# Optimization experiments

Hardware: AMD Instinct MI355X
Metric: run time of the kernel (lower is better)

The kernel has to match this reference:

```python
import jax, jax.numpy as jnp
import numpy as np

V, EMB, HID, ENC = 32000, 512, 1024, 1024
B, T, TB = 64, 512, 512
PAD = 0


def setup_inputs() -> dict:
    key = jax.random.key(0)
    kk = jax.random.split(key, 24)
    w = lambda k, s: jax.random.normal(k, s, dtype=jnp.float32) * 0.02
    a = lambda k, s: jax.random.normal(k, s, dtype=jnp.float32)
    emb_table = w(kk[0], (V, EMB)).at[PAD].set(0.0)  # padding_idx row zeroed
    IN = EMB + ENC + HID  # lstm input size
    return {
        "y": jax.random.randint(kk[1], (B,), 0, V),
        "h": a(kk[2], (B, HID)),
        "c": a(kk[3], (B, HID)),
        "enc_out": a(kk[4], (B, T, ENC)),
        "bwd_states": a(kk[5], (B, TB, HID)),
        "src_ids": jax.random.randint(kk[6], (B, T), 0, V),
        "src_mask": jnp.ones((B, T), dtype=jnp.int32),
        "emb_table": emb_table,
        "W_ih": w(kk[7], (4 * HID, IN)),
        "W_hh": w(kk[8], (4 * HID, HID)),
        "b_ih": jnp.zeros((4 * HID,), jnp.float32),
        "b_hh": jnp.zeros((4 * HID,), jnp.float32),
        "Wq_e": w(kk[9], (HID, HID)),
        "Wk_e": w(kk[10], (HID, ENC)),
        "v_e": w(kk[11], (HID,)),
        "Wq_b": w(kk[12], (HID, HID)),
        "Wk_b": w(kk[13], (HID, HID)),
        "v_b": w(kk[14], (HID,)),
        "Wp": w(kk[15], (V, HID)),
        "bp": jnp.zeros((V,), jnp.float32),
        "wc": w(kk[16], (ENC,)),
        "ws": w(kk[17], (HID,)),
        "wy": w(kk[18], (EMB,)),
        "pg_b": jnp.zeros((), jnp.float32),
    }


def _bahdanau(query, keys, Wq, Wk, v, mask=None):
    # query [B,H], keys [B,T,D] -> context [B,D], attn [B,T]
    q = query @ Wq.T                                  # [B,A]
    k = jnp.einsum("btd,ad->bta", keys, Wk)           # [B,T,A]
    e = jnp.einsum("bta,a->bt", jnp.tanh(q[:, None, :] + k), v)
    if mask is not None:
        e = jnp.where(mask == 0, jnp.finfo(e.dtype).min, e)
    attn = jax.nn.softmax(e, axis=-1)
    ctx = jnp.einsum("bt,btd->bd", attn, keys)
    return ctx, attn


def reference(y, h, c, enc_out, bwd_states, src_ids, src_mask, emb_table,
              W_ih, W_hh, b_ih, b_hh, Wq_e, Wk_e, v_e, Wq_b, Wk_b, v_b,
              Wp, bp, wc, ws, wy, pg_b):
    emb = emb_table[y]                                # [B,EMB]
    query = h                                         # state[0].squeeze(0)
    c_enc, attn_enc = _bahdanau(query, enc_out, Wq_e, Wk_e, v_e, src_mask)
    c_bwd, _ = _bahdanau(query, bwd_states, Wq_b, Wk_b, v_b)
    x = jnp.concatenate([emb, c_enc, c_bwd], axis=-1)  # [B,EMB+ENC+HID]
    gates = x @ W_ih.T + h @ W_hh.T + b_ih + b_hh      # [B,4H], torch order i,f,g,o
    i, f, g, o = jnp.split(gates, 4, axis=-1)
    c_new = jax.nn.sigmoid(f) * c + jax.nn.sigmoid(i) * jnp.tanh(g)
    h_new = jax.nn.sigmoid(o) * jnp.tanh(c_new)
    vocab_dist = jax.nn.softmax(h_new @ Wp.T + bp, axis=-1)  # [B,V]
    p_gen = jax.nn.sigmoid(c_enc @ wc + h_new @ ws + emb @ wy + pg_b)[:, None]
    p_vocab = p_gen * vocab_dist
    copy_mask = (src_ids < V).astype(vocab_dist.dtype)
    safe_ids = jnp.minimum(src_ids, V - 1)
    contrib = (1.0 - p_gen) * attn_enc * copy_mask     # [B,T]
    scatter = jax.vmap(lambda idx, val: jnp.zeros((V,), val.dtype).at[idx].add(val))(safe_ids, contrib)
    final_dist = p_vocab + scatter
    return final_dist, h_new, c_new
```

## Files before the change

kernel.cpp:

```cpp
#include <hip/hip_runtime.h>
#include <hip/hip_bf16.h>

#define VSZ   32000
#define EMBD  512
#define HIDD  1024
#define BB    64
#define TSEQ  512
#define G4    4096

typedef short bf16x8 __attribute__((ext_vector_type(8)));
typedef float f32x4  __attribute__((ext_vector_type(4)));

typedef __attribute__((address_space(3))) unsigned       lds_u32_t;
typedef __attribute__((address_space(1))) const unsigned glb_u32_t;
__device__ __forceinline__ void gload16(const void* g, void* l){
  __builtin_amdgcn_global_load_lds((glb_u32_t*)g, (lds_u32_t*)l, 16, 0, 0);
}

__device__ __forceinline__ float sigmoid_f(float x){ return 1.0f/(1.0f+__expf(-x)); }
__device__ __forceinline__ float fast_tanh(float x){
  float e = __expf(2.0f*x);
  return 1.0f - 2.0f*__builtin_amdgcn_rcpf(e + 1.0f);
}
__device__ __forceinline__ short f2bfs(float x){
  unsigned u = __float_as_uint(x);
  unsigned r = (u + 0x7FFFu + ((u>>16)&1u)) >> 16;
  return (short)r;
}
__device__ __forceinline__ float bf2f(short s){
  return __uint_as_float(((unsigned)(unsigned short)s) << 16);
}
__device__ __forceinline__ unsigned cvtpk(float a, float b){
  unsigned r;
  asm("v_cvt_pk_bf16_f32 %0, %1, %2" : "=v"(r) : "v"(a), "v"(b));
  return r;
}
__device__ __forceinline__ bf16x8 cvt8(float4 a, float4 b){
  union { unsigned u[4]; bf16x8 v; } o;
  o.u[0]=cvtpk(a.x,a.y); o.u[1]=cvtpk(a.z,a.w);
  o.u[2]=cvtpk(b.x,b.y); o.u[3]=cvtpk(b.z,b.w);
  return o.v;
}
__device__ __forceinline__ float wave_sum(float x){
  #pragma unroll
  for (int off=32; off>0; off>>=1) x += __shfl_xor(x, off);
  return x;
}
__device__ __forceinline__ float wave_max(float x){
  #pragma unroll
  for (int off=32; off>0; off>>=1) x = fmaxf(x, __shfl_xor(x, off));
  return x;
}

__global__ __launch_bounds__(256) void k_prep_all(
    const float* __restrict__ Wk_e, const float* __restrict__ Wk_b,
    const float* __restrict__ enc,  const float* __restrict__ bwd,
    const float* __restrict__ h,
    const float* __restrict__ tab,  const int* __restrict__ y,
    short* __restrict__ pk_e, short* __restrict__ pk_b,
    short* __restrict__ pkeys, short* __restrict__ xb){
  int bid = blockIdx.x;
  if (bid < 1024){
    const float* Wk = (bid < 512) ? Wk_e : Wk_b;
    short* dst      = (bid < 512) ? pk_e : pk_b;
    int id = (bid & 511)*256 + threadIdx.x;
    int a = id >> 7, g = id & 127;
    int gs = (g & ~7) | ((g & 7) ^ (a & 7));
    const float* src = Wk + (size_t)a*1024 + gs*8;
    float4 f0 = ((const float4*)src)[0], f1 = ((const float4*)src)[1];
    *(bf16x8*)(dst + (size_t)id*8) = cvt8(f0, f1);
  } else if (bid < 33792){
    int r = bid - 1024;
    int att = r >> 14;
    const float* src0 = att ? bwd : enc;
    int id = (r & 16383)*256 + threadIdx.x;
    int g = id & 127, bt = id >> 7;
    int t = bt & 511;
    int gs = (g & ~7) | ((g & 7) ^ (t & 7));
    const float* sp = src0 + (size_t)bt*1024 + gs*8;
    float4 f0 = ((const float4*)sp)[0], f1 = ((const float4*)sp)[1];
    *(bf16x8*)(pkeys + (((size_t)att*32768 + bt)*128 + g)*8) = cvt8(f0, f1);
  } else if (bid < 33824){
    int id = (bid - 33792)*256 + threadIdx.x;
    int b = id >> 7, d = (id & 127)*8;
    const float4* s = (const float4*)(h + (size_t)b*HIDD + d);
    *(bf16x8*)(xb + (size_t)b*3584 + 2560 + d) = cvt8(s[0], s[1]);
  } else {
    int id = (bid - 33824)*256 + threadIdx.x;
    int b = id >> 6, d = (id & 63)*8;
    const float* src = tab + (size_t)y[b]*EMBD + d;
    float4 f0 = ((const float4*)src)[0], f1 = ((const float4*)src)[1];
    *(bf16x8*)(xb + (size_t)b*3584 + d) = cvt8(f0, f1);
  }
}

__global__ __launch_bounds__(256) void k_mm64(
    const short* __restrict__ A0, int lda0, const float* __restrict__ B0, int ldb0, int K0, float* __restrict__ out0, int ldo0,
    const short* __restrict__ A1, int lda1, const float* __restrict__ B1, int ldb1, int K1, float* __restrict__ out1, int ldo1){
  const short* A; const float* B; float* out; int lda, ldb, K, ldo;
  if (blockIdx.z == 0){ A=A0; B=B0; out=out0; lda=lda0; ldb=ldb0; K=K0; ldo=ldo0; }
  else                { A=A1; B=B1; out=out1; lda=lda1; ldb=ldb1; K=K1; ldo=ldo1; }
  int tid = threadIdx.x, l = tid & 63, w = tid >> 6;
  int l15 = l & 15, l4 = l >> 4;
  int n0 = blockIdx.x*256 + w*64;
  int kper = K / gridDim.y;
  int dbeg = blockIdx.y * kper, dend = dbeg + kper;
  f32x4 acc[4][4];
  #pragma unroll
  for (int i=0;i<4;i++)
    #pragma unroll
    for (int j=0;j<4;j++)
      #pragma unroll
      for (int r=0;r<4;r++) acc[i][j][r]=0.f;
  for (int d0=dbeg; d0<dend; d0+=32){
    bf16x8 af[4];
    #pragma unroll
    for (int ms=0; ms<4; ms++)
      af[ms] = *(const bf16x8*)(A + (size_t)(ms*16 + l15)*lda + d0 + l4*8);
    bf16x8 bfr[4];
    #pragma unroll
    for (int ni=0; ni<4; ni++){
      const float* bp = B + (size_t)(n0 + ni*16 + l15)*ldb + d0 + l4*8;
      float4 f0 = ((const float4*)bp)[0], f1 = ((const float4*)bp)[1];
      bfr[ni] = cvt8(f0, f1);
    }
    #pragma unroll
    for (int ms=0; ms<4; ms++)
      #pragma unroll
      for (int ni=0; ni<4; ni++)
        acc[ms][ni] = __builtin_amdgcn_mfma_f32_16x16x32_bf16(af[ms], bfr[ni], acc[ms][ni], 0,0,0);
  }
  float* op = out + (size_t)blockIdx.y * 64 * ldo;
  #pragma unroll
  for (int ms=0; ms<4; ms++)
    #pragma unroll
    for (int ni=0; ni<4; ni++)
      #pragma unroll
      for (int r=0; r<4; r++){
        int m = ms*16 + l4*4 + r;
        op[(size_t)m*ldo + n0 + ni*16 + l15] = acc[ms][ni][r];
      }
}

__global__ __launch_bounds__(256,3) void k_energy(
    const short* __restrict__ pkeys,
    const short* __restrict__ pke, const short* __restrict__ pkb,
    const float* __restrict__ qpe, const float* __restrict__ qpb,
    const float* __restrict__ ve, const float* __restrict__ vb,
    float* __restrict__ ep_out){
  __shared__ short A_s[128*64];
  __shared__ short B_s[128*64];
  __shared__ float ebuf[2][128];

  int wg = blockIdx.x;
  int xcd = wg & 7, idx = wg >> 3;
  int tglob = xcd*64 + (idx >> 3);
  int A0 = idx & 7;
  int att = tglob >> 8;
  int tt  = tglob & 255;
  int b = tt >> 2, t0 = (tt & 3)*128;

  const short* pk = att ? pkb : pke;
  const float* qp = att ? qpb : qpe;
  const float* v  = att ? vb  : ve;

  int tid = threadIdx.x, l = tid & 63, w = tid >> 6;
  int l15 = l & 15, l4 = l >> 4;
  int wr = w >> 1, wc = w & 1;

  const char* asrc = (const char*)(pkeys + ((size_t)att*32768 + (size_t)b*512)*1024)
                   + (size_t)(t0 + w*32 + (l>>3))*2048 + (l&7)*16;
  const char* bsrc = (const char*)pk + (size_t)(A0*128 + w*32 + (l>>3))*2048 + (l&7)*16;

  f32x4 acc[4][4];
  #pragma unroll
  for (int i=0;i<4;i++)
    #pragma unroll
    for (int j=0;j<4;j++)
      #pragma unroll
      for (int r=0;r<4;r++) acc[i][j][r]=0.f;

  for (int c=0; c<16; ++c){
    if (c) __syncthreads();
    #pragma unroll
    for (int k=0;k<4;k++)
      gload16(asrc + (size_t)c*128 + (size_t)k*16384, (char*)A_s + w*4096 + k*1024);
    #pragma unroll
    for (int k=0;k<4;k++)
      gload16(bsrc + (size_t)c*128 + (size_t)k*16384, (char*)B_s + w*4096 + k*1024);
    __syncthreads();
    #pragma unroll
    for (int ks=0; ks<2; ks++){
      bf16x8 af[4], bf[4];
      #pragma unroll
      for (int ms=0; ms<4; ms++){
        int row = wr*64 + ms*16 + l15;
        af[ms] = *(const bf16x8*)((char*)A_s + row*128 + ((ks*64 + l4*16) ^ ((row&7)<<4)));
      }
      #pragma unroll
      for (int ni=0; ni<4; ni++){
        int row = wc*64 + ni*16 + l15;
        bf[ni] = *(const bf16x8*)((char*)B_s + row*128 + ((ks*64 + l4*16) ^ ((row&7)<<4)));
      }
      #pragma unroll
      for (int ms=0; ms<4; ms++)
        #pragma unroll
        for (int ni=0; ni<4; ni++)
          acc[ms][ni] = __builtin_amdgcn_mfma_f32_16x16x32_bf16(af[ms], bf[ni], acc[ms][ni], 0,0,0);
    }
  }

  float qv[4], vv[4];
  #pragma unroll
  for (int ni=0; ni<4; ni++){
    int a = A0*128 + wc*64 + ni*16 + l15;
    float q = 0.f;
    #pragma unroll
    for (int s=0; s<8; s++) q += qp[(size_t)s*65536 + (size_t)b*HIDD + a];
    qv[ni] = q;
    vv[ni] = v[a];
  }
  float es[16];
  #pragma unroll
  for (int ms=0; ms<4; ms++)
    #pragma unroll
    for (int r=0; r<4; r++){
      float s = 0.f;
      #pragma unroll
      for (int ni=0; ni<4; ni++)
        s += vv[ni]*fast_tanh(qv[ni] + acc[ms][ni][r]);
      es[ms*4+r] = s;
    }
  #pragma unroll
  for (int i=0;i<16;i++){
    float x = es[i];
    x += __shfl_xor(x,1); x += __shfl_xor(x,2);
    x += __shfl_xor(x,4); x += __shfl_xor(x,8);
    es[i] = x;
  }
  if (l15 == 0){
    #pragma unroll
    for (int ms=0; ms<4; ms++)
      #pragma unroll
      for (int r=0; r<4; r++)
        ebuf[wc][wr*64 + ms*16 + l4*4 + r] = es[ms*4+r];
  }
  __syncthreads();
  if (tid < 128)
    ep_out[(((size_t)att*8 + A0)*BB + b)*TSEQ + t0 + tid] = ebuf[0][tid] + ebuf[1][tid];
}

__global__ __launch_bounds__(256) void k_softmax_t(const float* __restrict__ ep,
                                                   const int* __restrict__ mask,
                                                   float* __restrict__ att_e,
                                                   float* __restrict__ att_b){
  int b = blockIdx.x, att = blockIdx.y;
  float* e = (att ? att_b : att_e) + (size_t)b*TSEQ;
  __shared__ float red[8];
  int tid = threadIdx.x, lane = tid & 63, w = tid >> 6;
  float v0 = 0.f, v1 = 0.f;
  #pragma unroll
  for (int i=0;i<8;i++){
    const float* p = ep + (((size_t)att*8 + i)*BB + b)*TSEQ;
    v0 += p[tid]; v1 += p[tid+256];
  }
  if (att==0){
    if (mask[(size_t)b*TSEQ + tid]==0)      v0 = -3.4e38f;
    if (mask[(size_t)b*TSEQ + tid+256]==0)  v1 = -3.4e38f;
  }
  float m = wave_max(fmaxf(v0, v1));
  if (lane==0) red[w] = m;
  __syncthreads();
  m = fmaxf(fmaxf(red[0],red[1]), fmaxf(red[2],red[3]));
  float x0 = __expf(v0-m), x1 = __expf(v1-m);
  float s = wave_sum(x0+x1);
  if (lane==0) red[4+w] = s;
  __syncthreads();
  s = red[4]+red[5]+red[6]+red[7];
  float inv = 1.0f/s;
  e[tid] = x0*inv; e[tid+256] = x1*inv;
}

__global__ __launch_bounds__(256) void k_ctx(const short* __restrict__ pkeys,
                                             const float* __restrict__ att_e,
                                             const float* __restrict__ att_b,
                                             float* __restrict__ ctxp){
  int b = blockIdx.x, sel = blockIdx.y, s = blockIdx.z;
  const short* base = pkeys + (((size_t)sel*32768) + (size_t)b*512 + s*64)*1024;
  const float* att  = (sel ? att_b : att_e) + (size_t)b*TSEQ + s*64;
  int g = threadIdx.x & 127, th = threadIdx.x >> 7;
  const short* rp = base + (size_t)th*32*1024;
  float acc[8];
  #pragma unroll
  for (int j=0;j<8;j++) acc[j]=0.f;
  for (int t=0;t<32;t++){
    float a = att[th*32 + t];
    int gg = (g & ~7) | ((g & 7) ^ (t & 7));
    bf16x8 kv = *(const bf16x8*)(rp + (size_t)t*1024 + gg*8);
    #pragma unroll
    for (int j=0;j<8;j++) acc[j] += a*bf2f(kv[j]);
  }
  float* o = ctxp + ((((size_t)sel*BB + b)*16) + s*2 + th)*1024 + g*8;
  float4 o0, o1;
  o0.x=acc[0]; o0.y=acc[1]; o0.z=acc[2]; o0.w=acc[3];
  o1.x=acc[4]; o1.y=acc[5]; o1.z=acc[6]; o1.w=acc[7];
  ((float4*)o)[0] = o0; ((float4*)o)[1] = o1;
}

__global__ __launch_bounds__(256) void k_ctxred(const float* __restrict__ ctxp,
                                                float* __restrict__ ctx_e,
                                                short* __restrict__ xb){
  int id = blockIdx.x*256 + threadIdx.x;
  int sel = id >> 16; int rem = id & 65535; int b = rem >> 10; int d = rem & 1023;
  const float* p = ctxp + (((size_t)sel*BB + b)*16)*1024 + d;
  float s = 0.f;
  #pragma unroll
  for (int i=0;i<16;i++) s += p[i*1024];
  if (sel==0) ctx_e[(size_t)b*HIDD + d] = s;
  xb[(size_t)b*3584 + 512 + sel*1024 + d] = f2bfs(s);
}

__global__ __launch_bounds__(256) void k_lstm(const float* __restrict__ gp,
                                              const float* __restrict__ b_ih,
                                              const float* __restrict__ b_hh,
                                              const float* __restrict__ c_old,
                                              float* __restrict__ out,
                                              short* __restrict__ hb){
  int id = blockIdx.x*256 + threadIdx.x;
  int b = id >> 10, j = id & 1023;
  size_t base = (size_t)b*G4;
  float gs[4];
  #pragma unroll
  for (int g=0; g<4; g++){
    int col = g*1024 + j;
    float s = b_ih[col] + b_hh[col];
    #pragma unroll
    for (int k=0;k<16;k++) s += gp[(size_t)k*(64*G4) + base + col];
    gs[g] = s;
  }
  float ig = sigmoid_f(gs[0]);
  float fg = sigmoid_f(gs[1]);
  float gg = tanhf(gs[2]);
  float og = sigmoid_f(gs[3]);
  float cn = fg*c_old[id] + ig*gg;
  float hn = og*tanhf(cn);
  out[(size_t)BB*VSZ + id] = hn;
  out[(size_t)BB*VSZ + (size_t)BB*HIDD + id] = cn;
  hb[id] = f2bfs(hn);
}

__global__ __launch_bounds__(256) void k_vocab2(const short* __restrict__ hb,
                                                const float* __restrict__ Wp,
                                                const float* __restrict__ bp,
                                                float* __restrict__ out){
  int tid = threadIdx.x, l = tid & 63, w = tid >> 6;
  int l15 = l & 15, l4 = l >> 4;
  int mh = w >> 1;
  int n0 = blockIdx.x*128 + (w&1)*64;
  f32x4 acc[2][4];
  #pragma unroll
  for (int i=0;i<2;i++)
    #pragma unroll
    for (int j=0;j<4;j++)
      #pragma unroll
      for (int r=0;r<4;r++) acc[i][j][r]=0.f;
  #pragma unroll 2
  for (int d0=0; d0<1024; d0+=32){
    bf16x8 af[2];
    #pragma unroll
    for (int ms=0; ms<2; ms++)
      af[ms] = *(const bf16x8*)(hb + (size_t)(mh*32 + ms*16 + l15)*1024 + d0 + l4*8);
    bf16x8 bfr[4];
    #pragma unroll
    for (int ni=0; ni<4; ni++){
      const float* bpp = Wp + (size_t)(n0 + ni*16 + l15)*1024 + d0 + l4*8;
      float4 f0 = ((const float4*)bpp)[0], f1 = ((const float4*)bpp)[1];
      bfr[ni] = cvt8(f0, f1);
    }
    #pragma unroll
    for (int ms=0; ms<2; ms++)
      #pragma unroll
      for (int ni=0; ni<4; ni++)
        acc[ms][ni] = __builtin_amdgcn_mfma_f32_16x16x32_bf16(af[ms], bfr[ni], acc[ms][ni], 0,0,0);
  }
  #pragma unroll
  for (int ms=0; ms<2; ms++)
    #pragma unroll
    for (int ni=0; ni<4; ni++)
      #pragma unroll
      for (int r=0; r<4; r++){
        int m = mh*32 + ms*16 + l4*4 + r;
        int n = n0 + ni*16 + l15;
        out[(size_t)m*VSZ + n] = acc[ms][ni][r] + bp[n];
      }
}

__global__ __launch_bounds__(256) void k_vred(const float* __restrict__ out,
                                              const float* __restrict__ ctxe,
                                              const float* __restrict__ tab,
                                              const int* __restrict__ y,
                                              const float* __restrict__ wc,
                                              const float* __restrict__ wsv,
                                              const float* __restrict__ wy,
                                              const float* __restrict__ pgb,
                                              float* __restrict__ vm,
                                              float* __restrict__ vs,
                                              float* __restrict__ pgen_ws){
  __shared__ float red[8];
  int b = blockIdx.x, seg = blockIdx.y;
  int tid = threadIdx.x, lane = tid & 63, w = tid >> 6;
  if (seg < 4){
    const float* row = out + (size_t)b*VSZ;
    int lo = seg*8000, hi = lo + 8000;
    float m = -3.4e38f;
    for (int i=lo+tid; i<hi; i+=256) m = fmaxf(m, row[i]);
    m = wave_max(m);
    if (lane==0) red[w] = m;
    __syncthreads();
    m = fmaxf(fmaxf(red[0],red[1]), fmaxf(red[2],red[3]));
    float s = 0.f;
    for (int i=lo+tid; i<hi; i+=256) s += __expf(row[i]-m);
    s = wave_sum(s);
    if (lane==0) red[4+w] = s;
    __syncthreads();
    if (tid==0){
      vm[b*4+seg] = m;
      vs[b*4+seg] = red[4]+red[5]+red[6]+red[7];
    }
  } else {
    const float* hn = out + (size_t)BB*VSZ + (size_t)b*HIDD;
    const float* emb = tab + (size_t)y[b]*EMBD;
    float acc = 0.f;
    #pragma unroll
    for (int i=0;i<4;i++){
      int d = i*256 + tid;
      acc += ctxe[(size_t)b*HIDD + d]*wc[d] + hn[d]*wsv[d];
    }
    #pragma unroll
    for (int i=0;i<2;i++){
      int d = i*256 + tid;
      acc += emb[d]*wy[d];
    }
    acc = wave_sum(acc);
    if (lane==0) red[w] = acc;
    __syncthreads();
    if (tid==0)
      pgen_ws[b] = sigmoid_f(red[0]+red[1]+red[2]+red[3] + pgb[0]);
  }
}

__global__ __launch_bounds__(256) void k_vscale(float* __restrict__ out,
                                                const float* __restrict__ vm,
                                                const float* __restrict__ vs,
                                                const float* __restrict__ pgen_ws){
  int b = blockIdx.x, seg = blockIdx.y;
  int tid = threadIdx.x;
  float m0=vm[b*4+0], m1=vm[b*4+1], m2=vm[b*4+2], m3=vm[b*4+3];
  float M = fmaxf(fmaxf(m0,m1), fmaxf(m2,m3));
  float S = vs[b*4+0]*__expf(m0-M) + vs[b*4+1]*__expf(m1-M)
          + vs[b*4+2]*__expf(m2-M) + vs[b*4+3]*__expf(m3-M);
  float scale = pgen_ws[b] / S;
  float* row = out + (size_t)b*VSZ;
  int lo = seg*8000, hi = lo + 8000;
  for (int i=lo+tid; i<hi; i+=256) row[i] = __expf(row[i]-M)*scale;
}

__global__ __launch_bounds__(256) void k_scatter(const int* __restrict__ src_ids,
                                                 const float* __restrict__ att_e,
                                                 const float* __restrict__ pgen_ws,
                                                 float* __restrict__ out){
  int id = blockIdx.x*256 + threadIdx.x;
  int b = id >> 9;
  float pg = pgen_ws[b];
  int sid = src_ids[id];
  float contrib = (1.0f - pg) * att_e[id] * (sid < VSZ ? 1.0f : 0.0f);
  int safe = sid < VSZ-1 ? sid : VSZ-1;
  atomicAdd(&out[(size_t)b*VSZ + safe], contrib);
}

extern "C" void kernel_launch(void* const* d_in, const int* in_sizes, int n_in,
                              void* d_out, int out_size, void* d_ws, size_t ws_size,
                              hipStream_t stream){
  const int*   y     = (const int*)d_in[0];
  const float* h     = (const float*)d_in[1];
  const float* c     = (const float*)d_in[2];
  const float* enc   = (const float*)d_in[3];
  const float* bwd   = (const float*)d_in[4];
  const int*   sids  = (const int*)d_in[5];
  const int*   smask = (const int*)d_in[6];
  const float* tab   = (const float*)d_in[7];
  const float* W_ih  = (const float*)d_in[8];
  const float* W_hh  = (const float*)d_in[9];
  const float* b_ih  = (const float*)d_in[10];
  const float* b_hh  = (const float*)d_in[11];
  const float* Wq_e  = (const float*)d_in[12];
  const float* Wk_e  = (const float*)d_in[13];
  const float* v_e   = (const float*)d_in[14];
  const float* Wq_b  = (const float*)d_in[15];
  const float* Wk_b  = (const float*)d_in[16];
  const float* v_b   = (const float*)d_in[17];
  const float* Wp    = (const float*)d_in[18];
  const float* bp    = (const float*)d_in[19];
  const float* wc    = (const float*)d_in[20];
  const float* wsv   = (const float*)d_in[21];
  const float* wy    = (const float*)d_in[22];
  const float* pgb   = (const float*)d_in[23];
  float* out = (float*)d_out;

  float* W = (float*)d_ws;
  float* ws_qpe  = W; W += 8*BB*HIDD;
  float* ws_qpb  = W; W += 8*BB*HIDD;
  float* ws_ep   = W; W += 2*8*BB*TSEQ;
  float* ws_atte = W; W += BB*TSEQ;
  float* ws_attb = W; W += BB*TSEQ;
  float* ws_ctxe = W; W += BB*HIDD;
  float* ws_ctxp = W; W += 2*BB*16*1024;
  float* ws_pgen = W; W += 64;
  float* ws_vm   = W; W += 256;
  float* ws_vs   = W; W += 256;
  float* ws_gp   = W; W += 16*BB*G4;
  short* xb      = (short*)W; W += (BB*3584)/2;
  short* hb      = (short*)W; W += (BB*HIDD)/2;
  short* pk_e    = (short*)W; W += (HIDD*HIDD)/2;
  short* pk_b    = (short*)W; W += (HIDD*HIDD)/2;
  short* pkeys   = (short*)W; W += (2*BB*TSEQ*HIDD)/2;

  k_prep_all<<<33840, 256, 0, stream>>>(Wk_e, Wk_b, enc, bwd, h, tab, y,
      pk_e, pk_b, pkeys, xb);
  k_mm64<<<dim3(4,8,2), 256, 0, stream>>>(
      xb+2560, 3584, Wq_e, 1024, 1024, ws_qpe, 1024,
      xb+2560, 3584, Wq_b, 1024, 1024, ws_qpb, 1024);
  k_energy<<<4096, 256, 0, stream>>>(pkeys, pk_e, pk_b,
      ws_qpe, ws_qpb, v_e, v_b, ws_ep);
  k_softmax_t<<<dim3(BB,2), 256, 0, stream>>>(ws_ep, smask, ws_atte, ws_attb);
  k_ctx<<<dim3(BB,2,8), 256, 0, stream>>>(pkeys, ws_atte, ws_attb, ws_ctxp);
  k_ctxred<<<512, 256, 0, stream>>>(ws_ctxp, ws_ctxe, xb);
  k_mm64<<<dim3(16,8,2), 256, 0, stream>>>(
      xb,      3584, W_ih, 2560, 2560, ws_gp,             G4,
      xb+2560, 3584, W_hh, 1024, 1024, ws_gp + 8*BB*G4,   G4);
  k_lstm<<<256, 256, 0, stream>>>(ws_gp, b_ih, b_hh, c, out, hb);
  k_vocab2<<<250, 256, 0, stream>>>(hb, Wp, bp, out);
  k_vred<<<dim3(BB,5), 256, 0, stream>>>(out, ws_ctxe, tab, y, wc, wsv, wy, pgb,
      ws_vm, ws_vs, ws_pgen);
  k_vscale<<<dim3(BB,4), 256, 0, stream>>>(out, ws_vm, ws_vs, ws_pgen);
  k_scatter<<<128, 256, 0, stream>>>(sids, ws_atte, ws_pgen, out);
}
```

Baseline: 367.7 us.

## Triple-buffer k_energy with async LDS loads and larger 256x128 tiles

Reworks the attention energy GEMM kernel to use 512-thread blocks covering 256 time rows by 128 attention columns, halving the grid. It adds a three-stage LDS ring fed by direct global-to-LDS loads, with explicit vmcnt waits and one barrier per k-step, so that loads for step k+2 overlap the MFMAs of step k. The goal is to hide global memory latency and to reuse each B tile across more rows. In exchange it uses far more LDS per block (about 144 KB) and runs one block per CU, which lowers occupancy and leaves latency hiding entirely to the hand-written pipeline.

```diff
diff --git a/kernel.cpp b/kernel.cpp
--- a/kernel.cpp
+++ b/kernel.cpp
@@ -142,23 +142,23 @@
       }
 }
 
-__global__ __launch_bounds__(256,3) void k_energy(
+__global__ __launch_bounds__(512,1) void k_energy(
     const short* __restrict__ pkeys,
     const short* __restrict__ pke, const short* __restrict__ pkb,
     const float* __restrict__ qpe, const float* __restrict__ qpb,
     const float* __restrict__ ve, const float* __restrict__ vb,
     float* __restrict__ ep_out){
-  __shared__ short A_s[128*64];
-  __shared__ short B_s[128*64];
-  __shared__ float ebuf[2][128];
+  __shared__ short A_all[3*256*64];
+  __shared__ short B_all[3*128*64];
+  __shared__ float ebuf[2][256];
 
   int wg = blockIdx.x;
   int xcd = wg & 7, idx = wg >> 3;
-  int tglob = xcd*64 + (idx >> 3);
-  int A0 = idx & 7;
-  int att = tglob >> 8;
-  int tt  = tglob & 255;
-  int b = tt >> 2, t0 = (tt & 3)*128;
+  int ntile = idx & 7;
+  int gmt = xcd*32 + (idx >> 3);
+  int att = gmt >> 7;
+  int b   = (gmt >> 1) & 63;
+  int t0  = (gmt & 1) * 256;
 
   const short* pk = att ? pkb : pke;
   const float* qp = att ? qpb : qpe;
@@ -166,11 +166,14 @@
 
   int tid = threadIdx.x, l = tid & 63, w = tid >> 6;
   int l15 = l & 15, l4 = l >> 4;
-  int wr = w >> 1, wc = w & 1;
+  int wm = w >> 1, wn = w & 1;
 
   const char* asrc = (const char*)(pkeys + ((size_t)att*32768 + (size_t)b*512)*1024)
                    + (size_t)(t0 + w*32 + (l>>3))*2048 + (l&7)*16;
-  const char* bsrc = (const char*)pk + (size_t)(A0*128 + w*32 + (l>>3))*2048 + (l&7)*16;
+  const char* bsrc = (const char*)pk + (size_t)(ntile*128 + w*16 + (l>>3))*2048 + (l&7)*16;
+
+  char* Ab = (char*)A_all;
+  char* Bb = (char*)B_all;
 
   f32x4 acc[4][4];
   #pragma unroll
@@ -180,40 +183,67 @@
       #pragma unroll
       for (int r=0;r<4;r++) acc[i][j][r]=0.f;
 
-  for (int c=0; c<16; ++c){
-    if (c) __syncthreads();
-    #pragma unroll
-    for (int k=0;k<4;k++)
-      gload16(asrc + (size_t)c*128 + (size_t)k*16384, (char*)A_s + w*4096 + k*1024);
-    #pragma unroll
-    for (int k=0;k<4;k++)
-      gload16(bsrc + (size_t)c*128 + (size_t)k*16384, (char*)B_s + w*4096 + k*1024);
-    __syncthreads();
-    #pragma unroll
-    for (int ks=0; ks<2; ks++){
-      bf16x8 af[4], bf[4];
-      #pragma unroll
-      for (int ms=0; ms<4; ms++){
-        int row = wr*64 + ms*16 + l15;
-        af[ms] = *(const bf16x8*)((char*)A_s + row*128 + ((ks*64 + l4*16) ^ ((row&7)<<4)));
-      }
-      #pragma unroll
-      for (int ni=0; ni<4; ni++){
-        int row = wc*64 + ni*16 + l15;
-        bf[ni] = *(const bf16x8*)((char*)B_s + row*128 + ((ks*64 + l4*16) ^ ((row&7)<<4)));
-      }
-      #pragma unroll
-      for (int ms=0; ms<4; ms++)
-        #pragma unroll
-        for (int ni=0; ni<4; ni++)
-          acc[ms][ni] = __builtin_amdgcn_mfma_f32_16x16x32_bf16(af[ms], bf[ni], acc[ms][ni], 0,0,0);
-    }
-  }
+#define STAGE(KT, BUF) { \
+    const char* as_ = asrc + (size_t)(KT)*128; \
+    char* ad_ = Ab + (BUF)*32768 + w*4096; \
+    gload16(as_,          ad_); \
+    gload16(as_ + 16384,  ad_ + 1024); \
+    gload16(as_ + 32768,  ad_ + 2048); \
+    gload16(as_ + 49152,  ad_ + 3072); \
+    const char* bs_ = bsrc + (size_t)(KT)*128; \
+    char* bd_ = Bb + (BUF)*16384 + w*2048; \
+    gload16(bs_,          bd_); \
+    gload16(bs_ + 16384,  bd_ + 1024); \
+  }
+
+#define MFMA_PHASE(BUF) { \
+    const char* Abase_ = Ab + (BUF)*32768; \
+    const char* Bbase_ = Bb + (BUF)*16384; \
+    _Pragma("unroll") \
+    for (int ks=0; ks<2; ks++){ \
+      bf16x8 af[4], bf[4]; \
+      _Pragma("unroll") \
+      for (int ms=0; ms<4; ms++){ \
+        int row = wm*64 + ms*16 + l15; \
+        af[ms] = *(const bf16x8*)(Abase_ + row*128 + ((ks*64 + l4*16) ^ ((row&7)<<4))); \
+      } \
+      _Pragma("unroll") \
+      for (int ni=0; ni<4; ni++){ \
+        int row = wn*64 + ni*16 + l15; \
+        bf[ni] = *(const bf16x8*)(Bbase_ + row*128 + ((ks*64 + l4*16) ^ ((row&7)<<4))); \
+      } \
+      _Pragma("unroll") \
+      for (int ms=0; ms<4; ms++) \
+        _Pragma("unroll") \
+        for (int ni=0; ni<4; ni++) \
+          acc[ms][ni] = __builtin_amdgcn_mfma_f32_16x16x32_bf16(af[ms], bf[ni], acc[ms][ni], 0,0,0); \
+    } }
+
+  STAGE(0, 0);
+  STAGE(1, 1);
+  asm volatile("s_waitcnt vmcnt(6)" ::: "memory");
+  __builtin_amdgcn_s_barrier();
+  __builtin_amdgcn_sched_barrier(0);
+
+  int cur = 0, stg = 2;
+  #pragma unroll 1
+  for (int kt = 0; kt < 16; ++kt){
+    if (kt < 14) STAGE(kt+2, stg);
+    MFMA_PHASE(cur);
+    if (kt <= 13) asm volatile("s_waitcnt vmcnt(6)" ::: "memory");
+    else          asm volatile("s_waitcnt vmcnt(0)" ::: "memory");
+    __builtin_amdgcn_s_barrier();
+    __builtin_amdgcn_sched_barrier(0);
+    cur = (cur==2) ? 0 : cur+1;
+    stg = (stg==2) ? 0 : stg+1;
+  }
+#undef STAGE
+#undef MFMA_PHASE
 
   float qv[4], vv[4];
   #pragma unroll
   for (int ni=0; ni<4; ni++){
-    int a = A0*128 + wc*64 + ni*16 + l15;
+    int a = ntile*128 + wn*64 + ni*16 + l15;
     float q = 0.f;
     #pragma unroll
     for (int s=0; s<8; s++) q += qp[(size_t)s*65536 + (size_t)b*HIDD + a];
@@ -243,11 +273,11 @@
     for (int ms=0; ms<4; ms++)
       #pragma unroll
       for (int r=0; r<4; r++)
-        ebuf[wc][wr*64 + ms*16 + l4*4 + r] = es[ms*4+r];
+        ebuf[wn][wm*64 + ms*16 + l4*4 + r] = es[ms*4+r];
   }
   __syncthreads();
-  if (tid < 128)
-    ep_out[(((size_t)att*8 + A0)*BB + b)*TSEQ + t0 + tid] = ebuf[0][tid] + ebuf[1][tid];
+  if (tid < 256)
+    ep_out[(((size_t)att*8 + ntile)*BB + b)*TSEQ + t0 + tid] = ebuf[0][tid] + ebuf[1][tid];
 }
 
 __global__ __launch_bounds__(256) void k_softmax_t(const float* __restrict__ ep,
@@ -530,7 +560,7 @@
   k_mm64<<<dim3(4,8,2), 256, 0, stream>>>(
       xb+2560, 3584, Wq_e, 1024, 1024, ws_qpe, 1024,
       xb+2560, 3584, Wq_b, 1024, 1024, ws_qpb, 1024);
-  k_energy<<<4096, 256, 0, stream>>>(pkeys, pk_e, pk_b,
+  k_energy<<<2048, 512, 0, stream>>>(pkeys, pk_e, pk_b,
       ws_qpe, ws_qpb, v_e, v_b, ws_ep);
   k_softmax_t<<<dim3(BB,2), 256, 0, stream>>>(ws_ep, smask, ws_atte, ws_attb);
   k_ctx<<<dim3(BB,2,8), 256, 0, stream>>>(pkeys, ws_atte, ws_attb, ws_ctxp);
```

New measurement: 449.8 us. 22.3% more time.
